# Kernel optimization log

Measured on AMD Instinct MI355X. Metric: run time of the kernel, lower is better.

The kernel has to match this reference:

```python
import jax, jax.numpy as jnp
import numpy as np

N = 8192
F_IN = 256
F_OUT = 128
ALPHA = 0.2  # leaky relu negative slope


def _leaky(x):
    return jnp.where(x >= 0, x, ALPHA * x)


def setup_inputs() -> dict:
    key = jax.random.key(0)
    ks = jax.random.split(key, 12)
    nodes = jax.random.normal(ks[0], (N, F_IN), dtype=jnp.float32)
    adj = (jax.random.uniform(ks[1], (N, N)) < 0.05).astype(jnp.float32)
    adj = jnp.maximum(adj, jnp.eye(N, dtype=jnp.float32))
    s = 0.02
    W1 = jax.random.normal(ks[2], (F_IN, F_OUT), dtype=jnp.float32) * s
    b1 = jnp.zeros((F_OUT,), jnp.float32)
    W2 = jax.random.normal(ks[3], (F_OUT, F_OUT), dtype=jnp.float32) * s
    b2 = jnp.zeros((F_OUT,), jnp.float32)
    W3 = jax.random.normal(ks[4], (F_OUT, F_OUT), dtype=jnp.float32) * s
    b3 = jnp.zeros((F_OUT,), jnp.float32)
    W4 = jax.random.normal(ks[5], (F_OUT, F_OUT), dtype=jnp.float32) * s
    b4 = jnp.zeros((F_OUT,), jnp.float32)
    a_w = jax.random.normal(ks[6], (2 * F_OUT,), dtype=jnp.float32) * s
    a_b = jnp.zeros((), jnp.float32)
    return {"nodes": nodes, "adj": adj, "W1": W1, "b1": b1, "W2": W2, "b2": b2,
            "W3": W3, "b3": b3, "W4": W4, "b4": b4, "a_w": a_w, "a_b": a_b}


def reference(nodes, adj, W1, b1, W2, b2, W3, b3, W4, b4, a_w, a_b):
    # 4-layer linear stack
    h = jax.nn.relu(nodes @ W1 + b1)
    h = jax.nn.relu(h @ W2 + b2)
    h = jax.nn.relu(h @ W3 + b3)
    h = h @ W4 + b4  # (N, F_OUT)
    # a([h_i, h_j]) is linear -> split into src/dst components instead of
    # materializing the (N, N, 2F) repeat+cat tensor; identical math.
    a1, a2 = a_w[:F_OUT], a_w[F_OUT:]
    s_src = h @ a1  # (N,)
    s_dst = h @ a2  # (N,)
    e = _leaky(s_src[:, None] + s_dst[None, :] + a_b)  # (N, N)
    e = jnp.where(adj >= 0.5, e, -jnp.inf)
    attention = jax.nn.softmax(e, axis=1)
    # dropout is identity in eval mode
    return _leaky(attention @ h)  # (N, F_OUT)
```

## Files before the change

### kernel.cpp

```cpp
#include <hip/hip_runtime.h>
#include <hip/hip_bf16.h>

#define N_NODES 8192
#define F_IN    256
#define F_OUT   128
#define QCAP    192

typedef float f4v __attribute__((ext_vector_type(4)));
typedef unsigned int u32;

__device__ __forceinline__ float leaky(float x) { return x >= 0.f ? x : 0.2f * x; }
__device__ __forceinline__ u32 bf16rn(float a) {
  const u32 u = __float_as_uint(a);
  return (u + 0x7FFFu + ((u >> 16) & 1u)) >> 16;
}
__device__ __forceinline__ u32 packbf(float a, float b) {
  return bf16rn(a) | (bf16rn(b) << 16);
}
__device__ __forceinline__ float bflo(u32 u) { return __uint_as_float(u << 16); }
__device__ __forceinline__ float bfhi(u32 u) { return __uint_as_float(u & 0xFFFF0000u); }

#define WAVE_LDS (8 * 256 + 8 * 128 + 8 * 128)

__device__ __forceinline__ void mlp_step4(const float* hbase, int stride, int k0,
                                          const float2 w[4], float acc[8][2]) {
#pragma unroll
  for (int r = 0; r < 8; ++r) {
    const float4 h4 = *(const float4*)(hbase + r * stride + k0);
    acc[r][0] += h4.x * w[0].x; acc[r][1] += h4.x * w[0].y;
    acc[r][0] += h4.y * w[1].x; acc[r][1] += h4.y * w[1].y;
    acc[r][0] += h4.z * w[2].x; acc[r][1] += h4.z * w[2].y;
    acc[r][0] += h4.w * w[3].x; acc[r][1] += h4.w * w[3].y;
  }
}

template <int K, int STRIDE>
__device__ __forceinline__ void mlp_layer(const float* __restrict__ W, int n0,
                                          const float* hbase, float acc[8][2]) {
#pragma unroll
  for (int r = 0; r < 8; ++r) { acc[r][0] = 0.f; acc[r][1] = 0.f; }
  float2 wA[4], wB[4];
#pragma unroll
  for (int kk = 0; kk < 4; ++kk)
    wA[kk] = *(const float2*)(W + (size_t)kk * F_OUT + n0);
#pragma unroll 1
  for (int k8 = 0; k8 < K / 8; ++k8) {
    const int kb = k8 * 8;
#pragma unroll
    for (int kk = 0; kk < 4; ++kk)
      wB[kk] = *(const float2*)(W + (size_t)(kb + 4 + kk) * F_OUT + n0);
    mlp_step4(hbase, STRIDE, kb, wA, acc);
    if (k8 + 1 < K / 8) {
#pragma unroll
      for (int kk = 0; kk < 4; ++kk)
        wA[kk] = *(const float2*)(W + (size_t)(kb + 8 + kk) * F_OUT + n0);
    }
    mlp_step4(hbase, STRIDE, kb + 4, wB, acc);
  }
}

__global__ __launch_bounds__(256) void mlp_fused(
    const float* __restrict__ nodes,
    const float* __restrict__ W1, const float* __restrict__ b1,
    const float* __restrict__ W2, const float* __restrict__ b2,
    const float* __restrict__ W3, const float* __restrict__ b3,
    const float* __restrict__ W4, const float* __restrict__ b4,
    const float* __restrict__ aw,
    u32* __restrict__ hb_out, float* __restrict__ ss, float* __restrict__ sd) {
  __shared__ float lds[4][WAVE_LDS];

  const int tid = threadIdx.x;
  const int w = tid >> 6;
  const int l = tid & 63;
  const int row0 = blockIdx.x * 32 + w * 8;
  const int n0 = 2 * l;

  float* A  = &lds[w][0];
  float* h1 = &lds[w][2048];
  float* h2 = &lds[w][2048 + 1024];

#pragma unroll
  for (int r = 0; r < 8; ++r) {
    const float4 v = *(const float4*)(nodes + (size_t)(row0 + r) * F_IN + l * 4);
    *(float4*)&A[r * 256 + l * 4] = v;
  }

  float acc[8][2];

  mlp_layer<256, 256>(W1, n0, A, acc);
  {
    const float2 bv = *(const float2*)(b1 + n0);
#pragma unroll
    for (int r = 0; r < 8; ++r) {
      float2 o = {fmaxf(acc[r][0] + bv.x, 0.f), fmaxf(acc[r][1] + bv.y, 0.f)};
      *(float2*)&h1[r * 128 + n0] = o;
    }
  }
  mlp_layer<128, 128>(W2, n0, h1, acc);
  {
    const float2 bv = *(const float2*)(b2 + n0);
#pragma unroll
    for (int r = 0; r < 8; ++r) {
      float2 o = {fmaxf(acc[r][0] + bv.x, 0.f), fmaxf(acc[r][1] + bv.y, 0.f)};
      *(float2*)&h2[r * 128 + n0] = o;
    }
  }
  mlp_layer<128, 128>(W3, n0, h2, acc);
  {
    const float2 bv = *(const float2*)(b3 + n0);
#pragma unroll
    for (int r = 0; r < 8; ++r) {
      float2 o = {fmaxf(acc[r][0] + bv.x, 0.f), fmaxf(acc[r][1] + bv.y, 0.f)};
      *(float2*)&h1[r * 128 + n0] = o;
    }
  }
  mlp_layer<128, 128>(W4, n0, h1, acc);
  {
    const float2 bv = *(const float2*)(b4 + n0);
#pragma unroll
    for (int r = 0; r < 8; ++r) { acc[r][0] += bv.x; acc[r][1] += bv.y; }
  }

  const float2 a1v = *(const float2*)(aw + n0);
  const float2 a2v = *(const float2*)(aw + F_OUT + n0);
#pragma unroll
  for (int r = 0; r < 8; ++r) {
    hb_out[(size_t)(row0 + r) * 64 + l] = packbf(acc[r][0], acc[r][1]);
    float s1 = acc[r][0] * a1v.x + acc[r][1] * a1v.y;
    float s2 = acc[r][0] * a2v.x + acc[r][1] * a2v.y;
#pragma unroll
    for (int o = 1; o < 64; o <<= 1) {
      s1 += __shfl_xor(s1, o, 64);
      s2 += __shfl_xor(s2, o, 64);
    }
    if (l == 0) { ss[row0 + r] = s1; sd[row0 + r] = s2; }
  }
}

__device__ __forceinline__ void compact4(const f4v v, int j0, int& base,
                                         unsigned long long lt, int* lc) {
  const bool hx = v.x >= 0.5f, hy = v.y >= 0.5f, hz = v.z >= 0.5f, hw = v.w >= 0.5f;
  const unsigned long long m0 = __ballot(hx);
  const unsigned long long m1 = __ballot(hy);
  const unsigned long long m2 = __ballot(hz);
  const unsigned long long m3 = __ballot(hw);
  const int t0 = __popcll(m0), t1 = __popcll(m1), t2 = __popcll(m2), t3 = __popcll(m3);
  if (hx) { const int p = base + __popcll(m0 & lt);                if (p < QCAP) lc[p] = j0; }
  if (hy) { const int p = base + t0 + __popcll(m1 & lt);           if (p < QCAP) lc[p] = j0 + 1; }
  if (hz) { const int p = base + t0 + t1 + __popcll(m2 & lt);      if (p < QCAP) lc[p] = j0 + 2; }
  if (hw) { const int p = base + t0 + t1 + t2 + __popcll(m3 & lt); if (p < QCAP) lc[p] = j0 + 3; }
  base += t0 + t1 + t2 + t3;
}

__global__ __launch_bounds__(256) void attn_row(const float* __restrict__ adj,
                                                const u32* __restrict__ hb,
                                                const float* __restrict__ s_src,
                                                const float* __restrict__ s_dst,
                                                const float* __restrict__ ab_ptr,
                                                float* __restrict__ out) {
  __shared__ int   lst[4][QCAP];
  __shared__ float accs[4][16][8];
  __shared__ float wss[4];

  const int tid = threadIdx.x;
  const int w = tid >> 6;
  const int lane = tid & 63;
  const int row = blockIdx.x;
  int* lc = lst[w];

  const float sbase = s_src[row] + ab_ptr[0];
  const f4v* arow = (const f4v*)(adj + (size_t)row * N_NODES) + w * 512;
  const uint4* hb4 = (const uint4*)hb;
  const unsigned long long lt = (1ull << lane) - 1ull;

  f4v a0 = __builtin_nontemporal_load(arow + lane);
  f4v a1 = __builtin_nontemporal_load(arow + 64 + lane);
  f4v a2 = __builtin_nontemporal_load(arow + 128 + lane);
  f4v a3 = __builtin_nontemporal_load(arow + 192 + lane);
  f4v a4 = __builtin_nontemporal_load(arow + 256 + lane);
  f4v a5 = __builtin_nontemporal_load(arow + 320 + lane);
  f4v a6 = __builtin_nontemporal_load(arow + 384 + lane);
  f4v a7 = __builtin_nontemporal_load(arow + 448 + lane);

  int base = 0;
  const int jb = w * 2048 + lane * 4;
  compact4(a0, jb,        base, lt, lc);
  compact4(a1, jb + 256,  base, lt, lc);
  compact4(a2, jb + 512,  base, lt, lc);
  compact4(a3, jb + 768,  base, lt, lc);
  compact4(a4, jb + 1024, base, lt, lc);
  compact4(a5, jb + 1280, base, lt, lc);
  compact4(a6, jb + 1536, base, lt, lc);
  compact4(a7, jb + 1792, base, lt, lc);

  const int n = (base < QCAP) ? base : QCAP;
  const int g4 = lane >> 4;
  const int q = lane & 15;
  float accv[8] = {};
  float ws = 0.f;
  for (int p = g4; p < n; p += 4) {
    const int j = lc[p];
    const float wgt = __expf(leaky(sbase + s_dst[j]));
    const uint4 hv = hb4[(size_t)j * 16 + q];
    ws += wgt;
    accv[0] += wgt * bflo(hv.x); accv[1] += wgt * bfhi(hv.x);
    accv[2] += wgt * bflo(hv.y); accv[3] += wgt * bfhi(hv.y);
    accv[4] += wgt * bflo(hv.z); accv[5] += wgt * bfhi(hv.z);
    accv[6] += wgt * bflo(hv.w); accv[7] += wgt * bfhi(hv.w);
  }

#pragma unroll
  for (int e = 0; e < 8; ++e) {
    accv[e] += __shfl_xor(accv[e], 16, 64);
    accv[e] += __shfl_xor(accv[e], 32, 64);
  }
  ws += __shfl_xor(ws, 16, 64);
  ws += __shfl_xor(ws, 32, 64);

  if (lane < 16) {
#pragma unroll
    for (int e = 0; e < 8; ++e) accs[w][q][e] = accv[e];
  }
  if (lane == 0) wss[w] = ws;
  __syncthreads();

  if (tid < 128) {
    const int q2 = tid >> 3, e = tid & 7;
    const float s = accs[0][q2][e] + accs[1][q2][e] + accs[2][q2][e] + accs[3][q2][e];
    const float wt = wss[0] + wss[1] + wss[2] + wss[3];
    out[(size_t)row * F_OUT + tid] = leaky(s / wt);
  }
}

extern "C" void kernel_launch(void* const* d_in, const int* in_sizes, int n_in,
                              void* d_out, int out_size, void* d_ws, size_t ws_size,
                              hipStream_t stream) {
  const float* nodes = (const float*)d_in[0];
  const float* adj   = (const float*)d_in[1];
  const float* W1    = (const float*)d_in[2];
  const float* b1    = (const float*)d_in[3];
  const float* W2    = (const float*)d_in[4];
  const float* b2    = (const float*)d_in[5];
  const float* W3    = (const float*)d_in[6];
  const float* b3    = (const float*)d_in[7];
  const float* W4    = (const float*)d_in[8];
  const float* b4    = (const float*)d_in[9];
  const float* aw    = (const float*)d_in[10];
  const float* ab    = (const float*)d_in[11];
  float* out = (float*)d_out;

  u32*  hb = (u32*)d_ws;
  float* ss = (float*)((char*)d_ws + (size_t)N_NODES * F_OUT * 2);
  float* sd = ss + N_NODES;

  mlp_fused<<<N_NODES / 32, 256, 0, stream>>>(nodes, W1, b1, W2, b2, W3, b3,
                                              W4, b4, aw, hb, ss, sd);
  attn_row<<<N_NODES, 256, 0, stream>>>(adj, hb, ss, sd, ab, out);
}
```

Measured before the change: 456.5 us.

## Overlap adjacency scan with MLP in one launch, gather in second kernel

Moves the adjacency-row compaction out of the attention kernel and into the MLP launch as extra blocks, so the dominant 256 MB adjacency stream runs concurrently with the MLP instead of after it. Neighbor lists and counts are written to global workspace and read back by a slimmer gather kernel. It also shrinks the MLP LDS footprint by aliasing buffers and unrolls the gather loop. The cost is an extra global write and read of the compacted index lists and more workspace.

```diff
diff --git a/kernel.cpp b/kernel.cpp
--- a/kernel.cpp
+++ b/kernel.cpp
@@ -4,6 +4,7 @@
 #define N_NODES 8192
 #define F_IN    256
 #define F_OUT   128
+#define NB_MLP  256
 #define QCAP    192
 
 typedef float f4v __attribute__((ext_vector_type(4)));
@@ -19,8 +20,6 @@
 }
 __device__ __forceinline__ float bflo(u32 u) { return __uint_as_float(u << 16); }
 __device__ __forceinline__ float bfhi(u32 u) { return __uint_as_float(u & 0xFFFF0000u); }
-
-#define WAVE_LDS (8 * 256 + 8 * 128 + 8 * 128)
 
 __device__ __forceinline__ void mlp_step4(const float* hbase, int stride, int k0,
                                           const float2 w[4], float acc[8][2]) {
@@ -56,84 +55,6 @@
         wA[kk] = *(const float2*)(W + (size_t)(kb + 8 + kk) * F_OUT + n0);
     }
     mlp_step4(hbase, STRIDE, kb + 4, wB, acc);
-  }
-}
-
-__global__ __launch_bounds__(256) void mlp_fused(
-    const float* __restrict__ nodes,
-    const float* __restrict__ W1, const float* __restrict__ b1,
-    const float* __restrict__ W2, const float* __restrict__ b2,
-    const float* __restrict__ W3, const float* __restrict__ b3,
-    const float* __restrict__ W4, const float* __restrict__ b4,
-    const float* __restrict__ aw,
-    u32* __restrict__ hb_out, float* __restrict__ ss, float* __restrict__ sd) {
-  __shared__ float lds[4][WAVE_LDS];
-
-  const int tid = threadIdx.x;
-  const int w = tid >> 6;
-  const int l = tid & 63;
-  const int row0 = blockIdx.x * 32 + w * 8;
-  const int n0 = 2 * l;
-
-  float* A  = &lds[w][0];
-  float* h1 = &lds[w][2048];
-  float* h2 = &lds[w][2048 + 1024];
-
-#pragma unroll
-  for (int r = 0; r < 8; ++r) {
-    const float4 v = *(const float4*)(nodes + (size_t)(row0 + r) * F_IN + l * 4);
-    *(float4*)&A[r * 256 + l * 4] = v;
-  }
-
-  float acc[8][2];
-
-  mlp_layer<256, 256>(W1, n0, A, acc);
-  {
-    const float2 bv = *(const float2*)(b1 + n0);
-#pragma unroll
-    for (int r = 0; r < 8; ++r) {
-      float2 o = {fmaxf(acc[r][0] + bv.x, 0.f), fmaxf(acc[r][1] + bv.y, 0.f)};
-      *(float2*)&h1[r * 128 + n0] = o;
-    }
-  }
-  mlp_layer<128, 128>(W2, n0, h1, acc);
-  {
-    const float2 bv = *(const float2*)(b2 + n0);
-#pragma unroll
-    for (int r = 0; r < 8; ++r) {
-      float2 o = {fmaxf(acc[r][0] + bv.x, 0.f), fmaxf(acc[r][1] + bv.y, 0.f)};
-      *(float2*)&h2[r * 128 + n0] = o;
-    }
-  }
-  mlp_layer<128, 128>(W3, n0, h2, acc);
-  {
-    const float2 bv = *(const float2*)(b3 + n0);
-#pragma unroll
-    for (int r = 0; r < 8; ++r) {
-      float2 o = {fmaxf(acc[r][0] + bv.x, 0.f), fmaxf(acc[r][1] + bv.y, 0.f)};
-      *(float2*)&h1[r * 128 + n0] = o;
-    }
-  }
-  mlp_layer<128, 128>(W4, n0, h1, acc);
-  {
-    const float2 bv = *(const float2*)(b4 + n0);
-#pragma unroll
-    for (int r = 0; r < 8; ++r) { acc[r][0] += bv.x; acc[r][1] += bv.y; }
-  }
-
-  const float2 a1v = *(const float2*)(aw + n0);
-  const float2 a2v = *(const float2*)(aw + F_OUT + n0);
-#pragma unroll
-  for (int r = 0; r < 8; ++r) {
-    hb_out[(size_t)(row0 + r) * 64 + l] = packbf(acc[r][0], acc[r][1]);
-    float s1 = acc[r][0] * a1v.x + acc[r][1] * a1v.y;
-    float s2 = acc[r][0] * a2v.x + acc[r][1] * a2v.y;
-#pragma unroll
-    for (int o = 1; o < 64; o <<= 1) {
-      s1 += __shfl_xor(s1, o, 64);
-      s2 += __shfl_xor(s2, o, 64);
-    }
-    if (l == 0) { ss[row0 + r] = s1; sd[row0 + r] = s2; }
   }
 }
 
@@ -152,13 +73,122 @@
   base += t0 + t1 + t2 + t3;
 }
 
-__global__ __launch_bounds__(256) void attn_row(const float* __restrict__ adj,
-                                                const u32* __restrict__ hb,
-                                                const float* __restrict__ s_src,
-                                                const float* __restrict__ s_dst,
-                                                const float* __restrict__ ab_ptr,
-                                                float* __restrict__ out) {
-  __shared__ int   lst[4][QCAP];
+__global__ __launch_bounds__(256) void mlp_scan(
+    const float* __restrict__ nodes, const float* __restrict__ adj,
+    const float* __restrict__ W1, const float* __restrict__ b1,
+    const float* __restrict__ W2, const float* __restrict__ b2,
+    const float* __restrict__ W3, const float* __restrict__ b3,
+    const float* __restrict__ W4, const float* __restrict__ b4,
+    const float* __restrict__ aw,
+    u32* __restrict__ hb_out, float* __restrict__ ss, float* __restrict__ sd,
+    int* __restrict__ qlist, int* __restrict__ qcnt) {
+  __shared__ float smem[4][2048];
+
+  const int tid = threadIdx.x;
+  const int w = tid >> 6;
+  const int lane = tid & 63;
+
+  if (blockIdx.x >= NB_MLP) {
+    const int row = blockIdx.x - NB_MLP;
+    int* lc = qlist + ((size_t)row * 4 + w) * QCAP;
+    const f4v* arow = (const f4v*)(adj + (size_t)row * N_NODES) + w * 512;
+    const unsigned long long lt = (1ull << lane) - 1ull;
+
+    f4v a0 = __builtin_nontemporal_load(arow + lane);
+    f4v a1 = __builtin_nontemporal_load(arow + 64 + lane);
+    f4v a2 = __builtin_nontemporal_load(arow + 128 + lane);
+    f4v a3 = __builtin_nontemporal_load(arow + 192 + lane);
+    f4v a4 = __builtin_nontemporal_load(arow + 256 + lane);
+    f4v a5 = __builtin_nontemporal_load(arow + 320 + lane);
+    f4v a6 = __builtin_nontemporal_load(arow + 384 + lane);
+    f4v a7 = __builtin_nontemporal_load(arow + 448 + lane);
+
+    int base = 0;
+    const int jb = w * 2048 + lane * 4;
+    compact4(a0, jb,        base, lt, lc);
+    compact4(a1, jb + 256,  base, lt, lc);
+    compact4(a2, jb + 512,  base, lt, lc);
+    compact4(a3, jb + 768,  base, lt, lc);
+    compact4(a4, jb + 1024, base, lt, lc);
+    compact4(a5, jb + 1280, base, lt, lc);
+    compact4(a6, jb + 1536, base, lt, lc);
+    compact4(a7, jb + 1792, base, lt, lc);
+    if (lane == 0) qcnt[row * 4 + w] = base;
+    return;
+  }
+
+  const int row0 = blockIdx.x * 32 + w * 8;
+  const int n0 = 2 * lane;
+
+  float* A  = &smem[w][0];
+  float* h1 = &smem[w][0];
+  float* h2 = &smem[w][1024];
+
+#pragma unroll
+  for (int r = 0; r < 8; ++r) {
+    const float4 v = *(const float4*)(nodes + (size_t)(row0 + r) * F_IN + lane * 4);
+    *(float4*)&A[r * 256 + lane * 4] = v;
+  }
+
+  float acc[8][2];
+
+  mlp_layer<256, 256>(W1, n0, A, acc);
+  {
+    const float2 bv = *(const float2*)(b1 + n0);
+#pragma unroll
+    for (int r = 0; r < 8; ++r) {
+      float2 o = {fmaxf(acc[r][0] + bv.x, 0.f), fmaxf(acc[r][1] + bv.y, 0.f)};
+      *(float2*)&h1[r * 128 + n0] = o;
+    }
+  }
+  mlp_layer<128, 128>(W2, n0, h1, acc);
+  {
+    const float2 bv = *(const float2*)(b2 + n0);
+#pragma unroll
+    for (int r = 0; r < 8; ++r) {
+      float2 o = {fmaxf(acc[r][0] + bv.x, 0.f), fmaxf(acc[r][1] + bv.y, 0.f)};
+      *(float2*)&h2[r * 128 + n0] = o;
+    }
+  }
+  mlp_layer<128, 128>(W3, n0, h2, acc);
+  {
+    const float2 bv = *(const float2*)(b3 + n0);
+#pragma unroll
+    for (int r = 0; r < 8; ++r) {
+      float2 o = {fmaxf(acc[r][0] + bv.x, 0.f), fmaxf(acc[r][1] + bv.y, 0.f)};
+      *(float2*)&h1[r * 128 + n0] = o;
+    }
+  }
+  mlp_layer<128, 128>(W4, n0, h1, acc);
+  {
+    const float2 bv = *(const float2*)(b4 + n0);
+#pragma unroll
+    for (int r = 0; r < 8; ++r) { acc[r][0] += bv.x; acc[r][1] += bv.y; }
+  }
+
+  const float2 a1v = *(const float2*)(aw + n0);
+  const float2 a2v = *(const float2*)(aw + F_OUT + n0);
+#pragma unroll
+  for (int r = 0; r < 8; ++r) {
+    hb_out[(size_t)(row0 + r) * 64 + lane] = packbf(acc[r][0], acc[r][1]);
+    float s1 = acc[r][0] * a1v.x + acc[r][1] * a1v.y;
+    float s2 = acc[r][0] * a2v.x + acc[r][1] * a2v.y;
+#pragma unroll
+    for (int o = 1; o < 64; o <<= 1) {
+      s1 += __shfl_xor(s1, o, 64);
+      s2 += __shfl_xor(s2, o, 64);
+    }
+    if (lane == 0) { ss[row0 + r] = s1; sd[row0 + r] = s2; }
+  }
+}
+
+__global__ __launch_bounds__(256) void attn_gather(const u32* __restrict__ hb,
+                                                   const int* __restrict__ qlist,
+                                                   const int* __restrict__ qcnt,
+                                                   const float* __restrict__ s_src,
+                                                   const float* __restrict__ s_dst,
+                                                   const float* __restrict__ ab_ptr,
+                                                   float* __restrict__ out) {
   __shared__ float accs[4][16][8];
   __shared__ float wss[4];
 
@@ -166,38 +196,18 @@
   const int w = tid >> 6;
   const int lane = tid & 63;
   const int row = blockIdx.x;
-  int* lc = lst[w];
 
   const float sbase = s_src[row] + ab_ptr[0];
-  const f4v* arow = (const f4v*)(adj + (size_t)row * N_NODES) + w * 512;
+  const int* lc = qlist + ((size_t)row * 4 + w) * QCAP;
   const uint4* hb4 = (const uint4*)hb;
-  const unsigned long long lt = (1ull << lane) - 1ull;
-
-  f4v a0 = __builtin_nontemporal_load(arow + lane);
-  f4v a1 = __builtin_nontemporal_load(arow + 64 + lane);
-  f4v a2 = __builtin_nontemporal_load(arow + 128 + lane);
-  f4v a3 = __builtin_nontemporal_load(arow + 192 + lane);
-  f4v a4 = __builtin_nontemporal_load(arow + 256 + lane);
-  f4v a5 = __builtin_nontemporal_load(arow + 320 + lane);
-  f4v a6 = __builtin_nontemporal_load(arow + 384 + lane);
-  f4v a7 = __builtin_nontemporal_load(arow + 448 + lane);
-
-  int base = 0;
-  const int jb = w * 2048 + lane * 4;
-  compact4(a0, jb,        base, lt, lc);
-  compact4(a1, jb + 256,  base, lt, lc);
-  compact4(a2, jb + 512,  base, lt, lc);
-  compact4(a3, jb + 768,  base, lt, lc);
-  compact4(a4, jb + 1024, base, lt, lc);
-  compact4(a5, jb + 1280, base, lt, lc);
-  compact4(a6, jb + 1536, base, lt, lc);
-  compact4(a7, jb + 1792, base, lt, lc);
-
-  const int n = (base < QCAP) ? base : QCAP;
+  const int cv = qcnt[row * 4 + w];
+  const int n = (cv < QCAP) ? cv : QCAP;
   const int g4 = lane >> 4;
   const int q = lane & 15;
+
   float accv[8] = {};
   float ws = 0.f;
+#pragma unroll 2
   for (int p = g4; p < n; p += 4) {
     const int j = lc[p];
     const float wgt = __expf(leaky(sbase + s_dst[j]));
@@ -249,11 +259,14 @@
   const float* ab    = (const float*)d_in[11];
   float* out = (float*)d_out;
 
-  u32*  hb = (u32*)d_ws;
-  float* ss = (float*)((char*)d_ws + (size_t)N_NODES * F_OUT * 2);
-  float* sd = ss + N_NODES;
-
-  mlp_fused<<<N_NODES / 32, 256, 0, stream>>>(nodes, W1, b1, W2, b2, W3, b3,
-                                              W4, b4, aw, hb, ss, sd);
-  attn_row<<<N_NODES, 256, 0, stream>>>(adj, hb, ss, sd, ab, out);
-}
+  char* wsb = (char*)d_ws;
+  u32*   hb    = (u32*)wsb;
+  float* ss    = (float*)(wsb + (size_t)N_NODES * F_OUT * 2);
+  float* sd    = ss + N_NODES;
+  int*   qcnt  = (int*)(sd + N_NODES);
+  int*   qlist = qcnt + N_NODES * 4;
+
+  mlp_scan<<<NB_MLP + N_NODES, 256, 0, stream>>>(
+      nodes, adj, W1, b1, W2, b2, W3, b3, W4, b4, aw, hb, ss, sd, qlist, qcnt);
+  attn_gather<<<N_NODES, 256, 0, stream>>>(hb, qlist, qcnt, ss, sd, ab, out);
+}
```

After: 444.8 us. 2.6% less time.
